# Performance work log

Hardware: AMD Instinct MI355X
Metric: run time of the kernel (lower is better)

The kernel has to match this reference:

```python
import jax, jax.numpy as jnp
import numpy as np

CHUNK = 128  # output-column chunk size; keeps the [N, Cin, CHUNK] abs-diff tile modest


def adder_fwd(x2, w):
    """AdderNet 'matmul': out[n, o] = -sum_i |x2[n, i] - w[i, o]|.
    Chunked over output columns to avoid materializing [N, Cin, Cout]."""
    N, Cin = x2.shape
    Cout = w.shape[1]
    nc = Cout // CHUNK
    wc = w.reshape(Cin, nc, CHUNK).transpose(1, 0, 2)  # [nc, Cin, CHUNK]

    def body(_, wci):
        # [N, Cin, CHUNK] tile -> reduce over Cin
        o = -jnp.abs(x2[:, :, None] - wci[None, :, :]).sum(axis=1)  # [N, CHUNK]
        return None, o

    _, outs = jax.lax.scan(body, None, wc)  # [nc, N, CHUNK]
    return outs.transpose(1, 0, 2).reshape(N, Cout)


def layer_norm(y, gamma, beta, eps=1e-5):
    m = y.mean(axis=-1, keepdims=True)
    v = y.var(axis=-1, keepdims=True)
    return (y - m) / jnp.sqrt(v + eps) * gamma + beta


def setup_inputs() -> dict:
    key = jax.random.key(0)
    ks = jax.random.split(key, 2)
    B, S, Cin, Cout = 2, 2048, 512, 512
    return {
        "x": jax.random.normal(ks[0], (B, S, Cin), jnp.float32),
        "weight": jax.random.normal(ks[1], (Cin, Cout), jnp.float32),
        "multi_bias_in": jnp.ones((1, Cin), jnp.float32),
        "multi_bias_out": jnp.ones((1, Cout), jnp.float32),
        "ln_gamma": jnp.ones((Cout,), jnp.float32),
        "ln_beta": jnp.zeros((Cout,), jnp.float32),
    }


def reference(x, weight, multi_bias_in, multi_bias_out, ln_gamma, ln_beta):
    batch_shape = x.shape[:-1]
    Cin, Cout = weight.shape
    xb = (x * multi_bias_in).reshape(-1, Cin)          # scale then flatten tokens
    o = adder_fwd(xb, weight).reshape(*batch_shape, Cout)
    o = o * multi_bias_out
    return layer_norm(o, ln_gamma, ln_beta)
```

## Files before the change

kernel.cpp:

```cpp
#include <hip/hip_runtime.h>


constexpr int BM = 64, BN = 64, BK = 32;
constexpr int TM = 4, TN = 4;

__global__ __launch_bounds__(256, 2)
void adder_gemm(const float* __restrict__ x, const float* __restrict__ w,
                const float* __restrict__ mbin, const float* __restrict__ mbout,
                float* __restrict__ out, int N, int Cin, int Cout) {
  __shared__ float xs[BK][BM + 1];
  __shared__ float ws[BK][BN];

  const int tid = threadIdx.x;
  const int tx = tid & 15;
  const int ty = tid >> 4;
  const int bm = blockIdx.x * BM;
  const int bn = blockIdx.y * BN;

  float acc[TM][TN];
  #pragma unroll
  for (int a = 0; a < TM; ++a)
    #pragma unroll
    for (int b = 0; b < TN; ++b) acc[a][b] = 0.f;

  for (int k0 = 0; k0 < Cin; k0 += BK) {
    #pragma unroll
    for (int it = 0; it < 2; ++it) {
      const int f = tid + it * 256;
      const int row = f >> 3;
      const int col = (f & 7) << 2;
      const float4 xv = *reinterpret_cast<const float4*>(&x[(size_t)(bm + row) * Cin + k0 + col]);
      const float4 bv = *reinterpret_cast<const float4*>(&mbin[k0 + col]);
      xs[col + 0][row] = xv.x * bv.x;
      xs[col + 1][row] = xv.y * bv.y;
      xs[col + 2][row] = xv.z * bv.z;
      xs[col + 3][row] = xv.w * bv.w;
      const int wrow = f >> 4;
      const int wcol = (f & 15) << 2;
      *reinterpret_cast<float4*>(&ws[wrow][wcol]) =
          *reinterpret_cast<const float4*>(&w[(size_t)(k0 + wrow) * Cout + bn + wcol]);
    }
    __syncthreads();

    #pragma unroll
    for (int kk = 0; kk < BK; ++kk) {
      float xr[TM];
      #pragma unroll
      for (int a = 0; a < TM; ++a) xr[a] = xs[kk][ty * TM + a];
      const float4 wv = *reinterpret_cast<const float4*>(&ws[kk][tx * TN]);
      const float wr[TN] = {wv.x, wv.y, wv.z, wv.w};
      #pragma unroll
      for (int a = 0; a < TM; ++a)
        #pragma unroll
        for (int b = 0; b < TN; ++b)
          acc[a][b] += fabsf(xr[a] - wr[b]);
    }
    __syncthreads();
  }

  const float4 mb = *reinterpret_cast<const float4*>(&mbout[bn + tx * TN]);
  #pragma unroll
  for (int a = 0; a < TM; ++a) {
    float4 o;
    o.x = -acc[a][0] * mb.x;
    o.y = -acc[a][1] * mb.y;
    o.z = -acc[a][2] * mb.z;
    o.w = -acc[a][3] * mb.w;
    *reinterpret_cast<float4*>(&out[(size_t)(bm + ty * TM + a) * Cout + bn + tx * TN]) = o;
  }
}

__global__ __launch_bounds__(256)
void ln_rows(float* __restrict__ out, const float* __restrict__ gamma,
             const float* __restrict__ beta, int N, int C) {
  const int wave = threadIdx.x >> 6;
  const int lane = threadIdx.x & 63;
  const int row = blockIdx.x * 4 + wave;
  if (row >= N) return;
  float* p = out + (size_t)row * C;

  float v[8];
  {
    const float4 a = *reinterpret_cast<const float4*>(&p[lane * 8]);
    const float4 b = *reinterpret_cast<const float4*>(&p[lane * 8 + 4]);
    v[0] = a.x; v[1] = a.y; v[2] = a.z; v[3] = a.w;
    v[4] = b.x; v[5] = b.y; v[6] = b.z; v[7] = b.w;
  }

  float s = 0.f;
  #pragma unroll
  for (int i = 0; i < 8; ++i) s += v[i];
  #pragma unroll
  for (int off = 32; off > 0; off >>= 1) s += __shfl_xor(s, off, 64);
  const float mean = s * (1.0f / 512.0f);

  float d2 = 0.f;
  #pragma unroll
  for (int i = 0; i < 8; ++i) {
    const float d = v[i] - mean;
    d2 += d * d;
  }
  #pragma unroll
  for (int off = 32; off > 0; off >>= 1) d2 += __shfl_xor(d2, off, 64);
  const float rstd = rsqrtf(d2 * (1.0f / 512.0f) + 1e-5f);

  const float4 g0 = *reinterpret_cast<const float4*>(&gamma[lane * 8]);
  const float4 g1 = *reinterpret_cast<const float4*>(&gamma[lane * 8 + 4]);
  const float4 b0 = *reinterpret_cast<const float4*>(&beta[lane * 8]);
  const float4 b1 = *reinterpret_cast<const float4*>(&beta[lane * 8 + 4]);
  const float gg[8] = {g0.x, g0.y, g0.z, g0.w, g1.x, g1.y, g1.z, g1.w};
  const float bb[8] = {b0.x, b0.y, b0.z, b0.w, b1.x, b1.y, b1.z, b1.w};

  float4 o0, o1;
  o0.x = (v[0] - mean) * rstd * gg[0] + bb[0];
  o0.y = (v[1] - mean) * rstd * gg[1] + bb[1];
  o0.z = (v[2] - mean) * rstd * gg[2] + bb[2];
  o0.w = (v[3] - mean) * rstd * gg[3] + bb[3];
  o1.x = (v[4] - mean) * rstd * gg[4] + bb[4];
  o1.y = (v[5] - mean) * rstd * gg[5] + bb[5];
  o1.z = (v[6] - mean) * rstd * gg[6] + bb[6];
  o1.w = (v[7] - mean) * rstd * gg[7] + bb[7];
  *reinterpret_cast<float4*>(&p[lane * 8]) = o0;
  *reinterpret_cast<float4*>(&p[lane * 8 + 4]) = o1;
}

extern "C" void kernel_launch(void* const* d_in, const int* in_sizes, int n_in,
                              void* d_out, int out_size, void* d_ws, size_t ws_size,
                              hipStream_t stream) {
  const float* x     = (const float*)d_in[0];
  const float* w     = (const float*)d_in[1];
  const float* mbin  = (const float*)d_in[2];
  const float* mbout = (const float*)d_in[3];
  const float* gamma = (const float*)d_in[4];
  const float* beta  = (const float*)d_in[5];
  float* out = (float*)d_out;

  const int Cin  = in_sizes[2];
  const int Cout = in_sizes[3];
  const int N    = in_sizes[0] / Cin;

  dim3 grid(N / BM, Cout / BN);
  adder_gemm<<<grid, 256, 0, stream>>>(x, w, mbin, mbout, out, N, Cin, Cout);
  ln_rows<<<dim3((N + 3) / 4), 256, 0, stream>>>(out, gamma, beta, N, Cout);
}
```

Before: 153.5 us.

## Double-buffer adder GEMM tiles, shrink to 4x2 per thread, remap LN blocks per XCD

The adder GEMM now double-buffers its shared-memory tiles, issuing global loads for the next K tile into registers before computing the current one and storing them afterwards, so only one barrier is needed per iteration. BN drops from 64 to 32 with a 4x2 micro-tile per thread, which doubles the block count and lowers register use, at the cost of less reuse per thread. The x tile is padded so it can be read as float4, and the layer-norm blocks are remapped so rows a GEMM block wrote are handled on the same XCD, aiming for L2 hits.

New measurement: 157.4 us. +2.5%, slower.

```diff
diff --git a/kernel.cpp b/kernel.cpp
--- a/kernel.cpp
+++ b/kernel.cpp
@@ -1,90 +1,108 @@
 #include <hip/hip_runtime.h>
 
 
-constexpr int BM = 64, BN = 64, BK = 32;
-constexpr int TM = 4, TN = 4;
+constexpr int BM = 64, BN = 32, BK = 32;
+constexpr int XPAD = 4;
 
 __global__ __launch_bounds__(256, 2)
 void adder_gemm(const float* __restrict__ x, const float* __restrict__ w,
                 const float* __restrict__ mbin, const float* __restrict__ mbout,
                 float* __restrict__ out, int N, int Cin, int Cout) {
-  __shared__ float xs[BK][BM + 1];
-  __shared__ float ws[BK][BN];
+  __shared__ float xs[2][BK][BM + XPAD];
+  __shared__ float wsh[2][BK][BN];
 
   const int tid = threadIdx.x;
   const int tx = tid & 15;
   const int ty = tid >> 4;
   const int bm = blockIdx.x * BM;
   const int bn = blockIdx.y * BN;
+  const int NT = Cin / BK;
 
-  float acc[TM][TN];
+  float acc[4][2];
   #pragma unroll
-  for (int a = 0; a < TM; ++a)
-    #pragma unroll
-    for (int b = 0; b < TN; ++b) acc[a][b] = 0.f;
+  for (int a = 0; a < 4; ++a) { acc[a][0] = 0.f; acc[a][1] = 0.f; }
 
-  for (int k0 = 0; k0 < Cin; k0 += BK) {
+  float4 px[2], pw;
+
+  auto LOADR = [&](int k0) {
     #pragma unroll
     for (int it = 0; it < 2; ++it) {
       const int f = tid + it * 256;
-      const int row = f >> 3;
-      const int col = (f & 7) << 2;
-      const float4 xv = *reinterpret_cast<const float4*>(&x[(size_t)(bm + row) * Cin + k0 + col]);
-      const float4 bv = *reinterpret_cast<const float4*>(&mbin[k0 + col]);
-      xs[col + 0][row] = xv.x * bv.x;
-      xs[col + 1][row] = xv.y * bv.y;
-      xs[col + 2][row] = xv.z * bv.z;
-      xs[col + 3][row] = xv.w * bv.w;
-      const int wrow = f >> 4;
-      const int wcol = (f & 15) << 2;
-      *reinterpret_cast<float4*>(&ws[wrow][wcol]) =
-          *reinterpret_cast<const float4*>(&w[(size_t)(k0 + wrow) * Cout + bn + wcol]);
+      const int xrow = f >> 3, xcol = (f & 7) << 2;
+      const float4 xv = *reinterpret_cast<const float4*>(&x[(size_t)(bm + xrow) * Cin + k0 + xcol]);
+      const float4 bv = *reinterpret_cast<const float4*>(&mbin[k0 + xcol]);
+      px[it] = make_float4(xv.x * bv.x, xv.y * bv.y, xv.z * bv.z, xv.w * bv.w);
     }
+    const int wrow = tid >> 3, wcol = (tid & 7) << 2;
+    pw = *reinterpret_cast<const float4*>(&w[(size_t)(k0 + wrow) * Cout + bn + wcol]);
+  };
+  auto STORES = [&](int buf) {
+    #pragma unroll
+    for (int it = 0; it < 2; ++it) {
+      const int f = tid + it * 256;
+      const int xrow = f >> 3, xcol = (f & 7) << 2;
+      xs[buf][xcol + 0][xrow] = px[it].x;
+      xs[buf][xcol + 1][xrow] = px[it].y;
+      xs[buf][xcol + 2][xrow] = px[it].z;
+      xs[buf][xcol + 3][xrow] = px[it].w;
+    }
+    const int wrow = tid >> 3, wcol = (tid & 7) << 2;
+    *reinterpret_cast<float4*>(&wsh[buf][wrow][wcol]) = pw;
+  };
+
+  LOADR(0);
+  STORES(0);
+  int cur = 0;
+  for (int t = 0; t < NT; ++t) {
+    if (t + 1 < NT) LOADR((t + 1) * BK);
     __syncthreads();
-
     #pragma unroll
     for (int kk = 0; kk < BK; ++kk) {
-      float xr[TM];
+      const float4 xv4 = *reinterpret_cast<const float4*>(&xs[cur][kk][ty * 4]);
+      const float2 wv  = *reinterpret_cast<const float2*>(&wsh[cur][kk][tx * 2]);
+      const float xr[4] = {xv4.x, xv4.y, xv4.z, xv4.w};
       #pragma unroll
-      for (int a = 0; a < TM; ++a) xr[a] = xs[kk][ty * TM + a];
-      const float4 wv = *reinterpret_cast<const float4*>(&ws[kk][tx * TN]);
-      const float wr[TN] = {wv.x, wv.y, wv.z, wv.w};
-      #pragma unroll
-      for (int a = 0; a < TM; ++a)
-        #pragma unroll
-        for (int b = 0; b < TN; ++b)
-          acc[a][b] += fabsf(xr[a] - wr[b]);
+      for (int a = 0; a < 4; ++a) {
+        acc[a][0] += fabsf(xr[a] - wv.x);
+        acc[a][1] += fabsf(xr[a] - wv.y);
+      }
     }
-    __syncthreads();
+    if (t + 1 < NT) STORES(cur ^ 1);
+    cur ^= 1;
   }
 
-  const float4 mb = *reinterpret_cast<const float4*>(&mbout[bn + tx * TN]);
+  const float2 mb = *reinterpret_cast<const float2*>(&mbout[bn + tx * 2]);
   #pragma unroll
-  for (int a = 0; a < TM; ++a) {
-    float4 o;
+  for (int a = 0; a < 4; ++a) {
+    float2 o;
     o.x = -acc[a][0] * mb.x;
     o.y = -acc[a][1] * mb.y;
-    o.z = -acc[a][2] * mb.z;
-    o.w = -acc[a][3] * mb.w;
-    *reinterpret_cast<float4*>(&out[(size_t)(bm + ty * TM + a) * Cout + bn + tx * TN]) = o;
+    *reinterpret_cast<float2*>(&out[(size_t)(bm + ty * 4 + a) * Cout + bn + tx * 2]) = o;
   }
 }
 
 __global__ __launch_bounds__(256)
 void ln_rows(float* __restrict__ out, const float* __restrict__ gamma,
              const float* __restrict__ beta, int N, int C) {
+  const int b = blockIdx.x;
+  const int xcd = b & 7;
+  const int idx = b >> 3;
+  const int bx  = xcd + 8 * (idx >> 4);
+  const int j   = idx & 15;
+  const int row0 = bx * 64 + j * 4;
+
   const int wave = threadIdx.x >> 6;
   const int lane = threadIdx.x & 63;
-  const int row = blockIdx.x * 4 + wave;
+  const int row = row0 + wave;
   if (row >= N) return;
   float* p = out + (size_t)row * C;
 
   float v[8];
   {
     const float4 a = *reinterpret_cast<const float4*>(&p[lane * 8]);
-    const float4 b = *reinterpret_cast<const float4*>(&p[lane * 8 + 4]);
+    const float4 bq = *reinterpret_cast<const float4*>(&p[lane * 8 + 4]);
     v[0] = a.x; v[1] = a.y; v[2] = a.z; v[3] = a.w;
-    v[4] = b.x; v[5] = b.y; v[6] = b.z; v[7] = b.w;
+    v[4] = bq.x; v[5] = bq.y; v[6] = bq.z; v[7] = bq.w;
   }
 
   float s = 0.f;
@@ -141,5 +159,5 @@
 
   dim3 grid(N / BM, Cout / BN);
   adder_gemm<<<grid, 256, 0, stream>>>(x, w, mbin, mbout, out, N, Cin, Cout);
-  ln_rows<<<dim3((N + 3) / 4), 256, 0, stream>>>(out, gamma, beta, N, Cout);
+  ln_rows<<<dim3(N / 4), 256, 0, stream>>>(out, gamma, beta, N, Cout);
 }
```
